# Kernel tuning notes

Hardware: AMD Instinct MI355X
Metric: run time of the kernel (lower is better)

## Reference

```python
import jax, jax.numpy as jnp
import numpy as np

TAU = 0.2
EPS = 1e-12  # matches torch F.normalize eps


def setup_inputs() -> dict:
    key = jax.random.key(0)
    k1, k2 = jax.random.split(key)
    N, D = 8192, 128
    h1 = jax.random.normal(k1, (N, D), dtype=jnp.float32)
    h2 = jax.random.normal(k2, (N, D), dtype=jnp.float32)
    return {"h1": h1, "h2": h2}


def _l2norm(x):
    # torch.nn.functional.normalize: x / max(||x||, eps)
    n = jnp.sqrt(jnp.sum(x * x, axis=1, keepdims=True))
    return x / jnp.maximum(n, EPS)


def _nt_xent(h1, h2):
    h1n = _l2norm(h1)
    h2n = _l2norm(h2)
    inter = jnp.exp((h1n @ h1n.T) / TAU)  # [N, N]
    intra = jnp.exp((h1n @ h2n.T) / TAU)  # [N, N]
    pos = jnp.diagonal(intra)
    neg = inter.sum(axis=1) + intra.sum(axis=1) - jnp.diagonal(inter)
    return -jnp.log(pos / neg)  # [N]


def reference(h1, h2):
    l1 = _nt_xent(h1, h2)
    l2 = _nt_xent(h2, h1)
    return jnp.mean((l1 + l2) * 0.5)
```

## Files before the change

kernel.cpp:

```cpp
#include <hip/hip_runtime.h>
#include <math.h>


constexpr int D = 128;
constexpr float E5 = 148.4131591025766f;

typedef __attribute__((ext_vector_type(16))) float f32x16;
typedef __attribute__((ext_vector_type(8)))  int   v8i;
typedef __attribute__((ext_vector_type(4)))  long  v4l;

__global__ __launch_bounds__(256) void normalize_kernel(
    const float2* __restrict__ h1, const float2* __restrict__ h2,
    unsigned short* __restrict__ P16, float* __restrict__ d12,
    float* __restrict__ rsum, float* __restrict__ out, int N)
{
    const float SC = sqrtf(5.0f * 1.44269504088896340736f);
    int gid = blockIdx.x * 256 + threadIdx.x;
    if (gid < 2 * N) rsum[gid] = 0.f;
    if (gid == 0) out[0] = 0.f;

    int row  = blockIdx.x * 4 + (threadIdx.x >> 6);
    int lane = threadIdx.x & 63;
    float2 u = h1[(size_t)row * 64 + lane];
    float2 w = h2[(size_t)row * 64 + lane];
    float ss1 = u.x * u.x + u.y * u.y;
    float ss2 = w.x * w.x + w.y * w.y;
    float s12 = u.x * w.x + u.y * w.y;
#pragma unroll
    for (int off = 32; off > 0; off >>= 1) {
        ss1 += __shfl_xor(ss1, off, 64);
        ss2 += __shfl_xor(ss2, off, 64);
        s12 += __shfl_xor(s12, off, 64);
    }
    float n1 = fmaxf(sqrtf(ss1), 1e-12f);
    float n2 = fmaxf(sqrtf(ss2), 1e-12f);
    float c1 = SC / n1, c2 = SC / n2;
    int p1 = __builtin_amdgcn_cvt_pk_fp8_f32(u.x * c1, u.y * c1, 0, false);
    int p2 = __builtin_amdgcn_cvt_pk_fp8_f32(w.x * c2, w.y * c2, 0, false);
    int r1 = row, r2 = N + row;
    int fi = lane >> 2, li = lane & 3;
    P16[(size_t)(((r1 >> 5) * 16 + fi) * 128) + (r1 & 31) * 4 + li] =
        (unsigned short)(p1 & 0xffff);
    P16[(size_t)(((r2 >> 5) * 16 + fi) * 128) + (r2 & 31) * 4 + li] =
        (unsigned short)(p2 & 0xffff);
    if (lane == 0) d12[row] = 5.f * s12 / (n1 * n2);
}

__device__ __forceinline__ v8i load_op(const unsigned char* p) {
    v4l t;
    t[0] = *(const long*)(p);
    t[1] = *(const long*)(p + 256);
    t[2] = *(const long*)(p + 512);
    t[3] = *(const long*)(p + 768);
    return __builtin_bit_cast(v8i, t);
}

__global__ __launch_bounds__(256, 2) void gram_mfma_kernel(
    const unsigned char* __restrict__ P, float* __restrict__ rsum, int N)
{
    const int I = blockIdx.x;
    int nT = 4, dBase = 0;
    if (blockIdx.y < 16) { dBase = blockIdx.y * 4; }
    else if (I < 64)     { nT = 1; dBase = 64; }
    else return;

    const int tx   = threadIdx.x;
    const int lane = tx & 63;
    const int l32  = lane & 31, lhi = lane >> 5;
    const int wi   = (tx >> 6) >> 1, wj = (tx >> 6) & 1;
    const int iBase = I * 128;
    const int fOff = lhi * 1024;

    v8i a[2][2];
#pragma unroll
    for (int st = 0; st < 2; ++st) {
        const unsigned char* xp =
            P + (size_t)(I * 4 + wi * 2 + st) * 4096 + fOff + l32 * 8;
#pragma unroll
        for (int kc = 0; kc < 2; ++kc)
            a[st][kc] = load_op(xp + kc * 2048);
    }

    float racc0[16], racc1[16];
#pragma unroll
    for (int r = 0; r < 16; ++r) { racc0[r] = 0.f; racc1[r] = 0.f; }
    float cpA[4] = {0.f, 0.f, 0.f, 0.f};
    float cpB[4] = {0.f, 0.f, 0.f, 0.f};

    const int j0 = wj * 64 + l32;
    const int j1 = j0 + 32;

    v8i b0[2], b1[2];
    {
        const int J0 = (I + dBase) & 127;
        const unsigned char* pb =
            P + (size_t)(J0 * 4 + wj * 2) * 4096 + fOff + l32 * 8;
#pragma unroll
        for (int kc = 0; kc < 2; ++kc) {
            b0[kc] = load_op(pb + kc * 2048);
            b1[kc] = load_op(pb + 4096 + kc * 2048);
        }
    }

#pragma unroll
    for (int t = 0; t < 4; ++t) {
        if (t >= nT) break;

        v8i n0[2], n1[2];
        const bool pf = (t + 1 < nT);
        if (pf) {
            const int Jn = (I + dBase + t + 1) & 127;
            const unsigned char* pb =
                P + (size_t)(Jn * 4 + wj * 2) * 4096 + fOff + l32 * 8;
#pragma unroll
            for (int kc = 0; kc < 2; ++kc) {
                n0[kc] = load_op(pb + kc * 2048);
                n1[kc] = load_op(pb + 4096 + kc * 2048);
            }
        }

        f32x16 acc00, acc01, acc10, acc11;
#pragma unroll
        for (int r = 0; r < 16; ++r) {
            acc00[r] = 0.f; acc01[r] = 0.f; acc10[r] = 0.f; acc11[r] = 0.f;
        }

#pragma unroll
        for (int kc = 0; kc < 2; ++kc) {
            acc00 = __builtin_amdgcn_mfma_scale_f32_32x32x64_f8f6f4(
                a[0][kc], b0[kc], acc00, 0, 0, 0, 127, 0, 127);
            acc10 = __builtin_amdgcn_mfma_scale_f32_32x32x64_f8f6f4(
                a[1][kc], b0[kc], acc10, 0, 0, 0, 127, 0, 127);
            acc01 = __builtin_amdgcn_mfma_scale_f32_32x32x64_f8f6f4(
                a[0][kc], b1[kc], acc01, 0, 0, 0, 127, 0, 127);
            acc11 = __builtin_amdgcn_mfma_scale_f32_32x32x64_f8f6f4(
                a[1][kc], b1[kc], acc11, 0, 0, 0, 127, 0, 127);
        }

        float c0 = 0.f, c1 = 0.f;
#pragma unroll
        for (int r = 0; r < 16; ++r) {
            float e00 = __builtin_amdgcn_exp2f(acc00[r]);
            float e01 = __builtin_amdgcn_exp2f(acc01[r]);
            float e10 = __builtin_amdgcn_exp2f(acc10[r]);
            float e11 = __builtin_amdgcn_exp2f(acc11[r]);
            racc0[r] += e00 + e01;
            racc1[r] += e10 + e11;
            c0 += e00 + e10;
            c1 += e01 + e11;
        }
        if ((dBase + t) != 0) { cpA[t] = c0; cpB[t] = c1; }

        if (pf) {
            b0[0] = n0[0]; b0[1] = n0[1];
            b1[0] = n1[0]; b1[1] = n1[1];
        }
    }

#pragma unroll
    for (int r = 0; r < 16; ++r) {
        float s0 = racc0[r], s1 = racc1[r];
#pragma unroll
        for (int off = 1; off < 32; off <<= 1) {
            s0 += __shfl_xor(s0, off, 64);
            s1 += __shfl_xor(s1, off, 64);
        }
        if (l32 == 0) {
            int rowm = (r & 3) + 8 * (r >> 2) + 4 * lhi;
            atomicAdd(&rsum[iBase + wi * 64 + rowm], s0);
            atomicAdd(&rsum[iBase + wi * 64 + 32 + rowm], s1);
        }
    }

#pragma unroll
    for (int t = 0; t < 4; ++t) {
        if (t >= nT) break;
        if ((dBase + t) == 0) continue;
        float c0 = cpA[t], c1 = cpB[t];
        c0 += __shfl_xor(c0, 32, 64);
        c1 += __shfl_xor(c1, 32, 64);
        if (lane < 32) {
            int jb = ((I + dBase + t) & 127) * 128;
            atomicAdd(&rsum[jb + j0], c0);
            atomicAdd(&rsum[jb + j1], c1);
        }
    }
}

__global__ __launch_bounds__(256) void loss_reduce_kernel(
    const float* __restrict__ rsum, const float* __restrict__ d12,
    float* __restrict__ out, int N)
{
    __shared__ float sm[256];
    float s = 0.f;
    for (int i = blockIdx.x * 256 + threadIdx.x; i < N; i += gridDim.x * 256) {
        float neg1 = rsum[i] - E5;
        float neg2 = rsum[N + i] - E5;
        s += 0.5f * (logf(neg1) + logf(neg2)) - d12[i];
    }
    sm[threadIdx.x] = s;
    __syncthreads();
    for (int w = 128; w > 0; w >>= 1) {
        if (threadIdx.x < w) sm[threadIdx.x] += sm[threadIdx.x + w];
        __syncthreads();
    }
    if (threadIdx.x == 0) atomicAdd(out, sm[0] / (float)N);
}

extern "C" void kernel_launch(void* const* d_in, const int* in_sizes, int n_in,
                              void* d_out, int out_size, void* d_ws, size_t ws_size,
                              hipStream_t stream) {
    const float* h1 = (const float*)d_in[0];
    const float* h2 = (const float*)d_in[1];
    const int N = in_sizes[0] / D;

    unsigned char* P = (unsigned char*)d_ws;
    float* rsum = (float*)(P + (size_t)2 * N * D);
    float* d12  = rsum + 2 * N;
    float* out  = (float*)d_out;

    normalize_kernel<<<N / 4, 256, 0, stream>>>(
        (const float2*)h1, (const float2*)h2,
        (unsigned short*)P, d12, rsum, out, N);

    dim3 grid(128, 17, 1);
    gram_mfma_kernel<<<grid, 256, 0, stream>>>(P, rsum, N);

    loss_reduce_kernel<<<32, 256, 0, stream>>>(rsum, d12, out, N);
}
```

Baseline: 118.1 us.

## Replace global atomics with LDS accumulation and per-slot partial sums

Row and column exp-sums in the Gram kernel are now gathered with shared-memory atomics per block. Each block then writes its sums to its own slot of a partial-sum buffer with 81 slots, instead of issuing global atomicAdds onto one rsum array. The loss kernel sums the 81 slots for each row, so the normalize kernel no longer has to zero rsum. This removes contention on global atomics, but it adds a roughly 5 MB write and a 5 MB read. That read is handled by a reduction kernel of only 32 blocks.

```diff
diff --git a/kernel.cpp b/kernel.cpp
--- a/kernel.cpp
+++ b/kernel.cpp
@@ -4,6 +4,7 @@
 
 constexpr int D = 128;
 constexpr float E5 = 148.4131591025766f;
+constexpr int NSLOT = 81;
 
 typedef __attribute__((ext_vector_type(16))) float f32x16;
 typedef __attribute__((ext_vector_type(8)))  int   v8i;
@@ -12,12 +13,10 @@
 __global__ __launch_bounds__(256) void normalize_kernel(
     const float2* __restrict__ h1, const float2* __restrict__ h2,
     unsigned short* __restrict__ P16, float* __restrict__ d12,
-    float* __restrict__ rsum, float* __restrict__ out, int N)
+    float* __restrict__ out, int N)
 {
     const float SC = sqrtf(5.0f * 1.44269504088896340736f);
-    int gid = blockIdx.x * 256 + threadIdx.x;
-    if (gid < 2 * N) rsum[gid] = 0.f;
-    if (gid == 0) out[0] = 0.f;
+    if (blockIdx.x * 256 + threadIdx.x == 0) out[0] = 0.f;
 
     int row  = blockIdx.x * 4 + (threadIdx.x >> 6);
     int lane = threadIdx.x & 63;
@@ -56,7 +55,7 @@
 }
 
 __global__ __launch_bounds__(256, 2) void gram_mfma_kernel(
-    const unsigned char* __restrict__ P, float* __restrict__ rsum, int N)
+    const unsigned char* __restrict__ P, float* __restrict__ part, int N)
 {
     const int I = blockIdx.x;
     int nT = 4, dBase = 0;
@@ -64,12 +63,23 @@
     else if (I < 64)     { nT = 1; dBase = 64; }
     else return;
 
+    __shared__ float ldsRow[128];
+    __shared__ float ldsCol[4][128];
+
     const int tx   = threadIdx.x;
     const int lane = tx & 63;
     const int l32  = lane & 31, lhi = lane >> 5;
     const int wi   = (tx >> 6) >> 1, wj = (tx >> 6) & 1;
     const int iBase = I * 128;
     const int fOff = lhi * 1024;
+
+    if (tx < 128) ldsRow[tx] = 0.f;
+    {
+        float* lc = &ldsCol[0][0];
+        lc[tx] = 0.f;
+        lc[tx + 256] = 0.f;
+    }
+    __syncthreads();
 
     v8i a[2][2];
 #pragma unroll
@@ -167,8 +177,8 @@
         }
         if (l32 == 0) {
             int rowm = (r & 3) + 8 * (r >> 2) + 4 * lhi;
-            atomicAdd(&rsum[iBase + wi * 64 + rowm], s0);
-            atomicAdd(&rsum[iBase + wi * 64 + 32 + rowm], s1);
+            atomicAdd(&ldsRow[wi * 64 + rowm], s0);
+            atomicAdd(&ldsRow[wi * 64 + 32 + rowm], s1);
         }
     }
 
@@ -180,23 +190,40 @@
         c0 += __shfl_xor(c0, 32, 64);
         c1 += __shfl_xor(c1, 32, 64);
         if (lane < 32) {
-            int jb = ((I + dBase + t) & 127) * 128;
-            atomicAdd(&rsum[jb + j0], c0);
-            atomicAdd(&rsum[jb + j1], c1);
+            atomicAdd(&ldsCol[t][j0], c0);
+            atomicAdd(&ldsCol[t][j1], c1);
+        }
+    }
+
+    __syncthreads();
+
+    if (tx < 128) {
+        const int y = blockIdx.y;
+        part[(size_t)y * (2 * N) + iBase + tx] = ldsRow[tx];
+#pragma unroll
+        for (int t = 0; t < 4; ++t) {
+            if (t >= nT) break;
+            const int J = (I + dBase + t) & 127;
+            const size_t slot = (y < 16) ? (size_t)(17 + y * 4 + t) : 16;
+            part[slot * (2 * N) + (size_t)J * 128 + tx] = ldsCol[t][tx];
         }
     }
 }
 
 __global__ __launch_bounds__(256) void loss_reduce_kernel(
-    const float* __restrict__ rsum, const float* __restrict__ d12,
+    const float* __restrict__ part, const float* __restrict__ d12,
     float* __restrict__ out, int N)
 {
     __shared__ float sm[256];
     float s = 0.f;
     for (int i = blockIdx.x * 256 + threadIdx.x; i < N; i += gridDim.x * 256) {
-        float neg1 = rsum[i] - E5;
-        float neg2 = rsum[N + i] - E5;
-        s += 0.5f * (logf(neg1) + logf(neg2)) - d12[i];
+        float r1 = 0.f, r2 = 0.f;
+#pragma unroll 9
+        for (int sl = 0; sl < NSLOT; ++sl) {
+            r1 += part[(size_t)sl * (2 * N) + i];
+            r2 += part[(size_t)sl * (2 * N) + N + i];
+        }
+        s += 0.5f * (logf(r1 - E5) + logf(r2 - E5)) - d12[i];
     }
     sm[threadIdx.x] = s;
     __syncthreads();
@@ -215,16 +242,16 @@
     const int N = in_sizes[0] / D;
 
     unsigned char* P = (unsigned char*)d_ws;
-    float* rsum = (float*)(P + (size_t)2 * N * D);
-    float* d12  = rsum + 2 * N;
+    float* part = (float*)(P + (size_t)2 * N * D);
+    float* d12  = part + (size_t)NSLOT * 2 * N;
     float* out  = (float*)d_out;
 
     normalize_kernel<<<N / 4, 256, 0, stream>>>(
         (const float2*)h1, (const float2*)h2,
-        (unsigned short*)P, d12, rsum, out, N);
+        (unsigned short*)P, d12, out, N);
 
     dim3 grid(128, 17, 1);
-    gram_mfma_kernel<<<grid, 256, 0, stream>>>(P, rsum, N);
-
-    loss_reduce_kernel<<<32, 256, 0, stream>>>(rsum, d12, out, N);
-}
+    gram_mfma_kernel<<<grid, 256, 0, stream>>>(P, part, N);
+
+    loss_reduce_kernel<<<32, 256, 0, stream>>>(part, d12, out, N);
+}
```

After: 124.1 us. 1.05x slower.
